# Kernel tuning notes

Measured on AMD Instinct MI355X. Metric: run time of the kernel, lower is better.

Reference implementation:

```python
import jax, jax.numpy as jnp
import numpy as np

C, P, E = 2048, 128, 2048          # clusters, max points per cluster, edges
N = C * P                          # total voxels
COORD_LO, COORD_HI = 1, 4          # coords_col


def setup_inputs() -> dict:
    key = jax.random.key(0)
    k1, k2, k3 = jax.random.split(key, 3)
    data = jax.random.normal(k1, (N, 8), dtype=jnp.float32)
    # disjoint clusters: contiguous index blocks of size P
    clusts = jnp.arange(N, dtype=jnp.int32).reshape(C, P)
    # valid point count per cluster in [64, 128]
    clust_sizes = jax.random.randint(k2, (C,), 64, P + 1, dtype=jnp.int32)
    edge_index = jax.random.randint(k3, (2, E), 0, C, dtype=jnp.int32)
    return {"data": data, "clusts": clusts, "clust_sizes": clust_sizes,
            "edge_index": edge_index}


def reference(data, clusts, clust_sizes, edge_index):
    # directed branch of ClustGeoEdgeEncoder (random edges -> undirected=False)
    coords = data[:, COORD_LO:COORD_HI]                 # [N, 3]
    pts = coords[clusts]                                # [C, P, 3]
    valid = jnp.arange(P)[None, :] < clust_sizes[:, None]  # [C, P]

    src, dst = edge_index[0], edge_index[1]
    x1, x2 = pts[src], pts[dst]                         # [E, P, 3]
    m1, m2 = valid[src], valid[dst]                     # [E, P]

    # pairwise squared Euclidean distances via gram trick (avoids [E,P,P,3])
    sq1 = jnp.sum(x1 * x1, axis=-1)                     # [E, P]
    sq2 = jnp.sum(x2 * x2, axis=-1)
    inner = jnp.einsum('epd,eqd->epq', x1, x2)          # [E, P, P]
    d2 = sq1[:, :, None] + sq2[:, None, :] - 2.0 * inner
    d2 = jnp.maximum(d2, 0.0)
    pair_ok = m1[:, :, None] & m2[:, None, :]
    d2 = jnp.where(pair_ok, d2, jnp.inf)

    # argmin over the flattened local distance matrix, as in the torch loop
    imin = jnp.argmin(d2.reshape(E, P * P), axis=1)
    i1, i2 = imin // P, imin % P
    er = jnp.arange(E)
    v1 = x1[er, i1]                                     # [E, 3] closest point in c1
    v2 = x2[er, i2]                                     # [E, 3] closest point in c2

    disp = v1 - v2
    lend = jnp.linalg.norm(disp, axis=-1)               # [E]
    safe = jnp.where(lend > 0, lend, 1.0)[:, None]
    disp = jnp.where(lend[:, None] > 0, disp / safe, disp)
    B = (disp[:, :, None] * disp[:, None, :]).reshape(E, 9)  # outer product

    return jnp.concatenate([v1, v2, disp, lend[:, None], B], axis=1)  # [E, 19]
```

## Files before the change

### kernel.cpp

```cpp
#include <hip/hip_runtime.h>
#include <math.h>

#define CC 2048
#define PP 128
#define EE 2048

__global__ __launch_bounds__(256) void clust_geo_edge_kernel(
    const float* __restrict__ data,
    const int*   __restrict__ clusts,
    const int*   __restrict__ clust_sizes,
    const int*   __restrict__ edge_index,
    float*       __restrict__ out)
{
    __shared__ float4 s1[PP];
    __shared__ float4 s2[PP];
    __shared__ float  red_v[4];
    __shared__ int    red_i[4];

    const int e = blockIdx.x;
    const int t = threadIdx.x;

    const int src = edge_index[e];
    const int dst = edge_index[EE + e];
    const int n1  = clust_sizes[src];
    const int n2  = clust_sizes[dst];

    {
        const int which = t >> 7;
        const int p = t & (PP - 1);
        const int c = which ? dst : src;
        const int n = which ? n2 : n1;
        const int pt = clusts[c * PP + p];
        float4 v = *reinterpret_cast<const float4*>(data + (size_t)pt * 8);
        const float x = v.y, y = v.z, z = v.w;
        const float sq = __fadd_rn(__fadd_rn(__fmul_rn(x, x), __fmul_rn(y, y)),
                                   __fmul_rn(z, z));
        const float w = (p < n) ? sq : INFINITY;
        float4 o;
        if (which) {
            o.x = -2.0f * x; o.y = -2.0f * y; o.z = -2.0f * z; o.w = w;
            s2[p] = o;
        } else {
            o.x = x; o.y = y; o.z = z; o.w = w;
            s1[p] = o;
        }
    }
    __syncthreads();

    const int qid  = t & 31;
    const int pgid = t >> 5;

    const float4 b0 = s2[qid];
    const float4 b1 = s2[qid + 32];
    const float4 b2 = s2[qid + 64];
    const float4 b3 = s2[qid + 96];

    float bv = INFINITY;
    int   br = 0;

    auto evalp = [&](const float4& A, const float4& B, const int r) {
        const float m2i = __fadd_rn(
            __fadd_rn(__fmul_rn(B.x, A.x), __fmul_rn(B.y, A.y)),
            __fmul_rn(B.z, A.z));
        const float d2 = __fadd_rn(__fadd_rn(A.w, B.w), m2i);
        const float nv = __builtin_amdgcn_fmed3f(d2, 0.0f, bv);
        if (nv < bv) br = r;
        bv = nv;
    };

    #pragma unroll
    for (int g = 0; g < 4; ++g) {
        const float4 a0 = s1[pgid + 8 * (4 * g + 0)];
        const float4 a1 = s1[pgid + 8 * (4 * g + 1)];
        const float4 a2 = s1[pgid + 8 * (4 * g + 2)];
        const float4 a3 = s1[pgid + 8 * (4 * g + 3)];
        evalp(a0, b0, (16 * g) + 0);  evalp(a0, b1, (16 * g) + 1);
        evalp(a0, b2, (16 * g) + 2);  evalp(a0, b3, (16 * g) + 3);
        evalp(a1, b0, (16 * g) + 4);  evalp(a1, b1, (16 * g) + 5);
        evalp(a1, b2, (16 * g) + 6);  evalp(a1, b3, (16 * g) + 7);
        evalp(a2, b0, (16 * g) + 8);  evalp(a2, b1, (16 * g) + 9);
        evalp(a2, b2, (16 * g) + 10); evalp(a2, b3, (16 * g) + 11);
        evalp(a3, b0, (16 * g) + 12); evalp(a3, b1, (16 * g) + 13);
        evalp(a3, b2, (16 * g) + 14); evalp(a3, b3, (16 * g) + 15);
    }

    const int mi = br >> 2;
    const int jj = br & 3;
    float best_v = bv;
    int   best_i = (pgid + 8 * mi) * PP + (qid + 32 * jj);

    #pragma unroll
    for (int off = 32; off > 0; off >>= 1) {
        const float ov = __shfl_down(best_v, off);
        const int   oi = __shfl_down(best_i, off);
        if (ov < best_v || (ov == best_v && oi < best_i)) {
            best_v = ov; best_i = oi;
        }
    }
    const int wave = t >> 6;
    if ((t & 63) == 0) { red_v[wave] = best_v; red_i[wave] = best_i; }
    __syncthreads();

    if (t == 0) {
        float fv = red_v[0]; int fi = red_i[0];
        #pragma unroll
        for (int w = 1; w < 4; ++w) {
            const float ov = red_v[w]; const int oi = red_i[w];
            if (ov < fv || (ov == fv && oi < fi)) { fv = ov; fi = oi; }
        }
        const int i1 = fi >> 7;
        const int i2 = fi & (PP - 1);
        const float4 A  = s1[i1];
        const float4 Bq = s2[i2];
        const float bx = __fmul_rn(Bq.x, -0.5f);
        const float by = __fmul_rn(Bq.y, -0.5f);
        const float bz = __fmul_rn(Bq.z, -0.5f);

        const float d0 = __fsub_rn(A.x, bx);
        const float d1 = __fsub_rn(A.y, by);
        const float d2 = __fsub_rn(A.z, bz);
        const float ss = __fadd_rn(__fadd_rn(__fmul_rn(d0, d0), __fmul_rn(d1, d1)),
                                   __fmul_rn(d2, d2));
        const float lend = __fsqrt_rn(ss);

        float u0 = d0, u1 = d1, u2 = d2;
        if (lend > 0.0f) {
            u0 = __fdiv_rn(d0, lend);
            u1 = __fdiv_rn(d1, lend);
            u2 = __fdiv_rn(d2, lend);
        }

        float* o = out + (size_t)e * 19;
        o[0] = A.x; o[1] = A.y; o[2] = A.z;
        o[3] = bx;  o[4] = by;  o[5] = bz;
        o[6] = u0;  o[7] = u1;  o[8] = u2;
        o[9] = lend;
        o[10] = __fmul_rn(u0, u0); o[11] = __fmul_rn(u0, u1); o[12] = __fmul_rn(u0, u2);
        o[13] = __fmul_rn(u1, u0); o[14] = __fmul_rn(u1, u1); o[15] = __fmul_rn(u1, u2);
        o[16] = __fmul_rn(u2, u0); o[17] = __fmul_rn(u2, u1); o[18] = __fmul_rn(u2, u2);
    }
}

extern "C" void kernel_launch(void* const* d_in, const int* in_sizes, int n_in,
                              void* d_out, int out_size, void* d_ws, size_t ws_size,
                              hipStream_t stream) {
    const float* data        = (const float*)d_in[0];
    const int*   clusts      = (const int*)d_in[1];
    const int*   clust_sizes = (const int*)d_in[2];
    const int*   edge_index  = (const int*)d_in[3];
    float*       out         = (float*)d_out;

    clust_geo_edge_kernel<<<EE, 256, 0, stream>>>(data, clusts, clust_sizes,
                                                  edge_index, out);
}
```

Measured before the change: 18.42 us.

## Process four edges per block with prefetched gathers and triple-buffered LDS

Each block now handles four edges instead of one. All global gathers for the four edges are issued up front into registers, and a triple-buffered shared-memory ring lets the next edge's data be staged while the current one is evaluated, leaving one barrier per edge. The aim is to hide gather latency and amortise block launch and setup cost. In exchange the grid shrinks to 512 blocks on a many-CU device, and register pressure and per-block serial work both rise.

```diff
diff --git a/kernel.cpp b/kernel.cpp
--- a/kernel.cpp
+++ b/kernel.cpp
@@ -4,6 +4,8 @@
 #define CC 2048
 #define PP 128
 #define EE 2048
+#define EPB 4
+#define NBLK (EE / EPB)
 
 __global__ __launch_bounds__(256) void clust_geo_edge_kernel(
     const float* __restrict__ data,
@@ -12,132 +14,151 @@
     const int*   __restrict__ edge_index,
     float*       __restrict__ out)
 {
-    __shared__ float4 s1[PP];
-    __shared__ float4 s2[PP];
-    __shared__ float  red_v[4];
-    __shared__ int    red_i[4];
+    __shared__ float4 sA[3][PP];
+    __shared__ float4 sB[3][PP];
+    __shared__ float  red_v[2][4];
+    __shared__ int    red_i[2][4];
 
-    const int e = blockIdx.x;
-    const int t = threadIdx.x;
+    const int t  = threadIdx.x;
+    const int e0 = blockIdx.x * EPB;
+    const int which = t >> 7;
+    const int p     = t & (PP - 1);
 
-    const int src = edge_index[e];
-    const int dst = edge_index[EE + e];
-    const int n1  = clust_sizes[src];
-    const int n2  = clust_sizes[dst];
+    int cown[EPB], nown[EPB];
+    #pragma unroll
+    for (int k = 0; k < EPB; ++k) {
+        const int s = edge_index[e0 + k];
+        const int d = edge_index[EE + e0 + k];
+        cown[k] = which ? d : s;
+        nown[k] = clust_sizes[cown[k]];
+    }
+    int pt[EPB];
+    #pragma unroll
+    for (int k = 0; k < EPB; ++k) pt[k] = clusts[cown[k] * PP + p];
+    float4 v[EPB];
+    #pragma unroll
+    for (int k = 0; k < EPB; ++k)
+        v[k] = *reinterpret_cast<const float4*>(data + (size_t)pt[k] * 8);
 
-    {
-        const int which = t >> 7;
-        const int p = t & (PP - 1);
-        const int c = which ? dst : src;
-        const int n = which ? n2 : n1;
-        const int pt = clusts[c * PP + p];
-        float4 v = *reinterpret_cast<const float4*>(data + (size_t)pt * 8);
-        const float x = v.y, y = v.z, z = v.w;
+    float4 stg[EPB];
+    #pragma unroll
+    for (int k = 0; k < EPB; ++k) {
+        const float x = v[k].y, y = v[k].z, z = v[k].w;
         const float sq = __fadd_rn(__fadd_rn(__fmul_rn(x, x), __fmul_rn(y, y)),
                                    __fmul_rn(z, z));
-        const float w = (p < n) ? sq : INFINITY;
-        float4 o;
+        const float w = (p < nown[k]) ? sq : INFINITY;
         if (which) {
-            o.x = -2.0f * x; o.y = -2.0f * y; o.z = -2.0f * z; o.w = w;
-            s2[p] = o;
+            stg[k] = make_float4(-2.0f * x, -2.0f * y, -2.0f * z, w);
         } else {
-            o.x = x; o.y = y; o.z = z; o.w = w;
-            s1[p] = o;
+            stg[k] = make_float4(x, y, z, w);
         }
     }
+
+    if (which) sB[0][p] = stg[0]; else sA[0][p] = stg[0];
     __syncthreads();
 
     const int qid  = t & 31;
     const int pgid = t >> 5;
 
-    const float4 b0 = s2[qid];
-    const float4 b1 = s2[qid + 32];
-    const float4 b2 = s2[qid + 64];
-    const float4 b3 = s2[qid + 96];
-
-    float bv = INFINITY;
-    int   br = 0;
-
-    auto evalp = [&](const float4& A, const float4& B, const int r) {
-        const float m2i = __fadd_rn(
-            __fadd_rn(__fmul_rn(B.x, A.x), __fmul_rn(B.y, A.y)),
-            __fmul_rn(B.z, A.z));
-        const float d2 = __fadd_rn(__fadd_rn(A.w, B.w), m2i);
-        const float nv = __builtin_amdgcn_fmed3f(d2, 0.0f, bv);
-        if (nv < bv) br = r;
-        bv = nv;
-    };
-
     #pragma unroll
-    for (int g = 0; g < 4; ++g) {
-        const float4 a0 = s1[pgid + 8 * (4 * g + 0)];
-        const float4 a1 = s1[pgid + 8 * (4 * g + 1)];
-        const float4 a2 = s1[pgid + 8 * (4 * g + 2)];
-        const float4 a3 = s1[pgid + 8 * (4 * g + 3)];
-        evalp(a0, b0, (16 * g) + 0);  evalp(a0, b1, (16 * g) + 1);
-        evalp(a0, b2, (16 * g) + 2);  evalp(a0, b3, (16 * g) + 3);
-        evalp(a1, b0, (16 * g) + 4);  evalp(a1, b1, (16 * g) + 5);
-        evalp(a1, b2, (16 * g) + 6);  evalp(a1, b3, (16 * g) + 7);
-        evalp(a2, b0, (16 * g) + 8);  evalp(a2, b1, (16 * g) + 9);
-        evalp(a2, b2, (16 * g) + 10); evalp(a2, b3, (16 * g) + 11);
-        evalp(a3, b0, (16 * g) + 12); evalp(a3, b1, (16 * g) + 13);
-        evalp(a3, b2, (16 * g) + 14); evalp(a3, b3, (16 * g) + 15);
-    }
-
-    const int mi = br >> 2;
-    const int jj = br & 3;
-    float best_v = bv;
-    int   best_i = (pgid + 8 * mi) * PP + (qid + 32 * jj);
-
-    #pragma unroll
-    for (int off = 32; off > 0; off >>= 1) {
-        const float ov = __shfl_down(best_v, off);
-        const int   oi = __shfl_down(best_i, off);
-        if (ov < best_v || (ov == best_v && oi < best_i)) {
-            best_v = ov; best_i = oi;
-        }
-    }
-    const int wave = t >> 6;
-    if ((t & 63) == 0) { red_v[wave] = best_v; red_i[wave] = best_i; }
-    __syncthreads();
-
-    if (t == 0) {
-        float fv = red_v[0]; int fi = red_i[0];
-        #pragma unroll
-        for (int w = 1; w < 4; ++w) {
-            const float ov = red_v[w]; const int oi = red_i[w];
-            if (ov < fv || (ov == fv && oi < fi)) { fv = ov; fi = oi; }
-        }
-        const int i1 = fi >> 7;
-        const int i2 = fi & (PP - 1);
-        const float4 A  = s1[i1];
-        const float4 Bq = s2[i2];
-        const float bx = __fmul_rn(Bq.x, -0.5f);
-        const float by = __fmul_rn(Bq.y, -0.5f);
-        const float bz = __fmul_rn(Bq.z, -0.5f);
-
-        const float d0 = __fsub_rn(A.x, bx);
-        const float d1 = __fsub_rn(A.y, by);
-        const float d2 = __fsub_rn(A.z, bz);
-        const float ss = __fadd_rn(__fadd_rn(__fmul_rn(d0, d0), __fmul_rn(d1, d1)),
-                                   __fmul_rn(d2, d2));
-        const float lend = __fsqrt_rn(ss);
-
-        float u0 = d0, u1 = d1, u2 = d2;
-        if (lend > 0.0f) {
-            u0 = __fdiv_rn(d0, lend);
-            u1 = __fdiv_rn(d1, lend);
-            u2 = __fdiv_rn(d2, lend);
+    for (int k = 0; k < EPB; ++k) {
+        const int cb = k % 3;
+        const int nb = (k + 1) % 3;
+        if (k + 1 < EPB) {
+            if (which) sB[nb][p] = stg[k + 1]; else sA[nb][p] = stg[k + 1];
         }
 
-        float* o = out + (size_t)e * 19;
-        o[0] = A.x; o[1] = A.y; o[2] = A.z;
-        o[3] = bx;  o[4] = by;  o[5] = bz;
-        o[6] = u0;  o[7] = u1;  o[8] = u2;
-        o[9] = lend;
-        o[10] = __fmul_rn(u0, u0); o[11] = __fmul_rn(u0, u1); o[12] = __fmul_rn(u0, u2);
-        o[13] = __fmul_rn(u1, u0); o[14] = __fmul_rn(u1, u1); o[15] = __fmul_rn(u1, u2);
-        o[16] = __fmul_rn(u2, u0); o[17] = __fmul_rn(u2, u1); o[18] = __fmul_rn(u2, u2);
+        const float4 b0 = sB[cb][qid];
+        const float4 b1 = sB[cb][qid + 32];
+        const float4 b2 = sB[cb][qid + 64];
+        const float4 b3 = sB[cb][qid + 96];
+
+        float bv = INFINITY;
+        int   br = 0;
+
+        auto evalp = [&](const float4& A, const float4& B, const int r) {
+            const float m2i = __fadd_rn(
+                __fadd_rn(__fmul_rn(B.x, A.x), __fmul_rn(B.y, A.y)),
+                __fmul_rn(B.z, A.z));
+            const float d2 = __fadd_rn(__fadd_rn(A.w, B.w), m2i);
+            const float nv = __builtin_amdgcn_fmed3f(d2, 0.0f, bv);
+            if (nv < bv) br = r;
+            bv = nv;
+        };
+
+        #pragma unroll
+        for (int g = 0; g < 4; ++g) {
+            const float4 a0 = sA[cb][pgid + 8 * (4 * g + 0)];
+            const float4 a1 = sA[cb][pgid + 8 * (4 * g + 1)];
+            const float4 a2 = sA[cb][pgid + 8 * (4 * g + 2)];
+            const float4 a3 = sA[cb][pgid + 8 * (4 * g + 3)];
+            evalp(a0, b0, (16 * g) + 0);  evalp(a0, b1, (16 * g) + 1);
+            evalp(a0, b2, (16 * g) + 2);  evalp(a0, b3, (16 * g) + 3);
+            evalp(a1, b0, (16 * g) + 4);  evalp(a1, b1, (16 * g) + 5);
+            evalp(a1, b2, (16 * g) + 6);  evalp(a1, b3, (16 * g) + 7);
+            evalp(a2, b0, (16 * g) + 8);  evalp(a2, b1, (16 * g) + 9);
+            evalp(a2, b2, (16 * g) + 10); evalp(a2, b3, (16 * g) + 11);
+            evalp(a3, b0, (16 * g) + 12); evalp(a3, b1, (16 * g) + 13);
+            evalp(a3, b2, (16 * g) + 14); evalp(a3, b3, (16 * g) + 15);
+        }
+
+        const int mi = br >> 2;
+        const int jj = br & 3;
+        float best_v = bv;
+        int   best_i = (pgid + 8 * mi) * PP + (qid + 32 * jj);
+
+        #pragma unroll
+        for (int off = 32; off > 0; off >>= 1) {
+            const float ov = __shfl_down(best_v, off);
+            const int   oi = __shfl_down(best_i, off);
+            if (ov < best_v || (ov == best_v && oi < best_i)) {
+                best_v = ov; best_i = oi;
+            }
+        }
+        const int wave = t >> 6;
+        const int par  = k & 1;
+        if ((t & 63) == 0) { red_v[par][wave] = best_v; red_i[par][wave] = best_i; }
+        __syncthreads();
+
+        if (t == 0) {
+            float fv = red_v[par][0]; int fi = red_i[par][0];
+            #pragma unroll
+            for (int w = 1; w < 4; ++w) {
+                const float ov = red_v[par][w]; const int oi = red_i[par][w];
+                if (ov < fv || (ov == fv && oi < fi)) { fv = ov; fi = oi; }
+            }
+            const int i1 = fi >> 7;
+            const int i2 = fi & (PP - 1);
+            const float4 A  = sA[cb][i1];
+            const float4 Bq = sB[cb][i2];
+            const float bx = __fmul_rn(Bq.x, -0.5f);
+            const float by = __fmul_rn(Bq.y, -0.5f);
+            const float bz = __fmul_rn(Bq.z, -0.5f);
+
+            const float d0 = __fsub_rn(A.x, bx);
+            const float d1 = __fsub_rn(A.y, by);
+            const float d2 = __fsub_rn(A.z, bz);
+            const float ss = __fadd_rn(
+                __fadd_rn(__fmul_rn(d0, d0), __fmul_rn(d1, d1)),
+                __fmul_rn(d2, d2));
+            const float lend = __fsqrt_rn(ss);
+
+            float u0 = d0, u1 = d1, u2 = d2;
+            if (lend > 0.0f) {
+                u0 = __fdiv_rn(d0, lend);
+                u1 = __fdiv_rn(d1, lend);
+                u2 = __fdiv_rn(d2, lend);
+            }
+
+            float* o = out + (size_t)(e0 + k) * 19;
+            o[0] = A.x; o[1] = A.y; o[2] = A.z;
+            o[3] = bx;  o[4] = by;  o[5] = bz;
+            o[6] = u0;  o[7] = u1;  o[8] = u2;
+            o[9] = lend;
+            o[10] = __fmul_rn(u0, u0); o[11] = __fmul_rn(u0, u1); o[12] = __fmul_rn(u0, u2);
+            o[13] = __fmul_rn(u1, u0); o[14] = __fmul_rn(u1, u1); o[15] = __fmul_rn(u1, u2);
+            o[16] = __fmul_rn(u2, u0); o[17] = __fmul_rn(u2, u1); o[18] = __fmul_rn(u2, u2);
+        }
     }
 }
 
@@ -150,6 +171,6 @@
     const int*   edge_index  = (const int*)d_in[3];
     float*       out         = (float*)d_out;
 
-    clust_geo_edge_kernel<<<EE, 256, 0, stream>>>(data, clusts, clust_sizes,
-                                                  edge_index, out);
+    clust_geo_edge_kernel<<<NBLK, 256, 0, stream>>>(data, clusts, clust_sizes,
+                                                    edge_index, out);
 }
```

Result: slower. 20.11 us (+9.2%).
